# Kernel optimization log

Measured on AMD Instinct MI355X. Metric: run time of the kernel, lower is better.

Reference implementation:

```python
import jax, jax.numpy as jnp
import numpy as np

TAU = 2.0
THR = 1.0
ALPHA = 10.0
FLOW_SCALE = 16.0  # 2 ** flow_scale_pow2 (=4)
DECAY = 1.0 - 1.0 / TAU


def conv2d(x, w, b=None, stride=1, pad=0):
    # x: [N,C,H,W], w: [O,I,kh,kw]
    out = jax.lax.conv_general_dilated(
        x, w, (stride, stride), [(pad, pad), (pad, pad)],
        dimension_numbers=('NCHW', 'OIHW', 'NCHW'))
    if b is not None:
        out = out + b[None, :, None, None]
    return out


@jax.custom_vjp
def spike(v):
    return (v > 0).astype(v.dtype)

def _spike_fwd(v):
    return (v > 0).astype(v.dtype), v

def _spike_bwd(v, g):
    s = jax.nn.sigmoid(ALPHA * v)
    return (g * ALPHA * s * (1.0 - s),)

spike.defvjp(_spike_fwd, _spike_bwd)


def lif(x, w, b, mem, stride, pad):
    """Conv + leaky-integrate-fire with soft reset. mem init 0 -> first step mem=cur."""
    cur = conv2d(x, w, b, stride, pad)
    mem = mem * DECAY + cur
    s = spike(mem - THR)
    mem = mem - s * THR
    return s, mem


def up2(x):
    return jnp.repeat(jnp.repeat(x, 2, axis=2), 2, axis=3)


def forward(x, w_e1, b_e1, w_e2, b_e2, w_e3, b_e3, w_d3, b_d3,
            w_d2, b_d2, w_d1, b_d1, w_skip2, w_skip1, w_flow, b_flow):
    N, T, C, H, W = x.shape
    bc = w_e1.shape[0]  # base_ch = 32
    z = lambda c, h, w: jnp.zeros((N, c, h, w), x.dtype)
    init = (
        z(bc, H // 2, W // 2),      # mem_e1
        z(2 * bc, H // 4, W // 4),  # mem_e2
        z(4 * bc, H // 8, W // 8),  # mem_e3
        z(2 * bc, H // 4, W // 4),  # mem_d3
        z(bc, H // 2, W // 2),      # mem_d2
        z(bc, H, W),                # mem_d1
        z(bc, H // 2, W // 2),      # mean_e1 (zeros + /(t+1) rule == None-init)
        z(2 * bc, H // 4, W // 4),  # mean_e2
        z(2, H, W),                 # flow_mean
    )

    def step(carry, inp):
        t, xt = inp
        m1, m2, m3, md3, md2, md1, me1, me2, fm = carry
        s1, m1 = lif(xt, w_e1, b_e1, m1, 2, 2)
        s2, m2 = lif(s1, w_e2, b_e2, m2, 2, 1)
        s3, m3 = lif(s2, w_e3, b_e3, m3, 2, 1)
        tf = (t + 1).astype(xt.dtype)
        me1 = me1 + (s1 - me1) / tf
        me2 = me2 + (s2 - me2) / tf
        d3, md3 = lif(up2(s3), w_d3, b_d3, md3, 1, 1)
        d3 = d3 + conv2d(me2, w_skip2)
        d2, md2 = lif(up2(d3), w_d2, b_d2, md2, 1, 1)
        d2 = d2 + conv2d(me1, w_skip1)
        d1, md1 = lif(up2(d2), w_d1, b_d1, md1, 1, 1)
        flow = conv2d(d1, w_flow, b_flow, 1, 1) * FLOW_SCALE
        fm = fm + (flow - fm) / tf
        return (m1, m2, m3, md3, md2, md1, me1, me2, fm), flow

    _, flows = jax.lax.scan(step, init, (jnp.arange(T), jnp.moveaxis(x, 1, 0)))
    return flows[-1]  # return_last_flow=True -> flow of final timestep [N,2,H,W]


def setup_inputs() -> dict:
    key = jax.random.key(0)
    ks = jax.random.split(key, 16)
    N, T, H, W, bc = 4, 8, 256, 256, 32

    def w(k, o, i, kh, kw):
        return jax.random.normal(k, (o, i, kh, kw), jnp.float32) / np.sqrt(i * kh * kw)

    return {
        'x': jax.random.uniform(ks[0], (N, T, 2, H, W), jnp.float32),
        'w_e1': w(ks[1], bc, 2, 5, 5), 'b_e1': jnp.zeros((bc,), jnp.float32),
        'w_e2': w(ks[2], 2 * bc, bc, 3, 3), 'b_e2': jnp.zeros((2 * bc,), jnp.float32),
        'w_e3': w(ks[3], 4 * bc, 2 * bc, 3, 3), 'b_e3': jnp.zeros((4 * bc,), jnp.float32),
        'w_d3': w(ks[4], 2 * bc, 4 * bc, 3, 3), 'b_d3': jnp.zeros((2 * bc,), jnp.float32),
        'w_d2': w(ks[5], bc, 2 * bc, 3, 3), 'b_d2': jnp.zeros((bc,), jnp.float32),
        'w_d1': w(ks[6], bc, bc, 3, 3), 'b_d1': jnp.zeros((bc,), jnp.float32),
        'w_skip2': w(ks[7], 2 * bc, 2 * bc, 1, 1),
        'w_skip1': w(ks[8], bc, bc, 1, 1),
        'w_flow': w(ks[9], 2, bc, 3, 3), 'b_flow': jnp.zeros((2,), jnp.float32),
    }


def reference(x, w_e1, b_e1, w_e2, b_e2, w_e3, b_e3, w_d3, b_d3,
              w_d2, b_d2, w_d1, b_d1, w_skip2, w_skip1, w_flow, b_flow):
    return forward(x, w_e1, b_e1, w_e2, b_e2, w_e3, b_e3, w_d3, b_d3,
                   w_d2, b_d2, w_d1, b_d1, w_skip2, w_skip1, w_flow, b_flow)
```

## Files before the change

### kernel.cpp

```cpp
#include <hip/hip_runtime.h>
#include <cstdint>
#include <cstddef>


static constexpr float THRc   = 1.0f;
static constexpr float DECAYc = 0.5f;

__global__ __launch_bounds__(256) void prep_collapse(const float* __restrict__ w,
                                                     float* __restrict__ wc, int pairs)
{
    int idx = blockIdx.x * 256 + threadIdx.x;
    if (idx >= pairs) return;
    float a[3][3];
#pragma unroll
    for (int i = 0; i < 3; ++i)
#pragma unroll
        for (int j = 0; j < 3; ++j) a[i][j] = w[idx * 9 + i * 3 + j];
    float rs[2][2][3];
#pragma unroll
    for (int kx = 0; kx < 3; ++kx) {
        rs[0][0][kx] = a[0][kx];
        rs[0][1][kx] = a[1][kx] + a[2][kx];
        rs[1][0][kx] = a[0][kx] + a[1][kx];
        rs[1][1][kx] = a[2][kx];
    }
#pragma unroll
    for (int py = 0; py < 2; ++py)
#pragma unroll
        for (int px = 0; px < 2; ++px)
#pragma unroll
            for (int r = 0; r < 2; ++r) {
                float c0, c1;
                if (px == 0) { c0 = rs[py][r][0];               c1 = rs[py][r][1] + rs[py][r][2]; }
                else         { c0 = rs[py][r][0] + rs[py][r][1]; c1 = rs[py][r][2]; }
                wc[idx * 16 + ((py * 2 + px) * 2 + r) * 2 + 0] = c0;
                wc[idx * 16 + ((py * 2 + px) * 2 + r) * 2 + 1] = c1;
            }
}

template<int IC, int ICC, int OC, int SIH, int SIW, int CPT, int YPB, int OCT, int SKIP_IC>
__global__ __launch_bounds__(256) void dec_conv(
    const float* __restrict__ in,
    const float* __restrict__ wc,
    const float* __restrict__ bias,
    float* __restrict__ mem,
    float* __restrict__ out,
    const float* __restrict__ skip_in,
    const float* __restrict__ skip_w)
{
    constexpr int LPT  = SIW / CPT;
    static_assert(LPT * YPB == 64, "wave must tile the band");
    static_assert((ICC & (ICC - 1)) == 0, "ICC pow2");
    constexpr int OC_B = 4 * OCT;
    constexpr int NOCB = OC / OC_B;
    constexpr int NYB  = SIH / YPB;
    constexpr int SP   = SIW + 8;
    constexpr int SR   = YPB + 2;
    constexpr int OH   = 2 * SIH, OW = 2 * SIW;
    constexpr int NCH  = IC / ICC;
    constexpr int W4   = SIW / 4;

    __shared__ float sb[SR][ICC][SP];

    int b = blockIdx.x;
    const int ocb = b % NOCB; b /= NOCB;
    const int yb  = b % NYB;  b /= NYB;
    const int n   = b;
    const int y0  = yb * YPB;

    const int lane = threadIdx.x & 63;
    const int wav  = threadIdx.x >> 6;
    const int cl   = lane % LPT;
    const int yp   = lane / LPT;
    const int c0   = cl * CPT;
    const int y    = y0 + yp;

    const int oc0 = __builtin_amdgcn_readfirstlane(ocb * OC_B + wav * OCT);

    for (int f = threadIdx.x; f < SR * ICC * 2; f += 256) {
        int side = f & 1;
        int t    = f >> 1;
        int ic   = t & (ICC - 1);
        int r    = t / ICC;
        sb[r][ic][side ? (SIW + 4) : 3] = 0.0f;
    }

    float acc[OCT][2][2 * CPT];
#pragma unroll
    for (int j = 0; j < OCT; ++j) {
        float bv = bias[oc0 + j];
#pragma unroll
        for (int py = 0; py < 2; ++py)
#pragma unroll
            for (int q = 0; q < 2 * CPT; ++q) acc[j][py][q] = bv;
    }

    const float* inn = in + (size_t)n * IC * SIH * SIW;

    for (int ch = 0; ch < NCH; ++ch) {
        __syncthreads();
        const float* inb = inn + (size_t)ch * ICC * SIH * SIW;
        constexpr int SLOTS = SR * ICC * W4;
        for (int f = threadIdx.x; f < SLOTS; f += 256) {
            int c4 = f & (W4 - 1);
            int t  = f / W4;
            int ic = t & (ICC - 1);
            int r  = t / ICC;
            int sy = y0 - 1 + r;
            float4 v = make_float4(0.f, 0.f, 0.f, 0.f);
            if (sy >= 0 && sy < SIH)
                v = *reinterpret_cast<const float4*>(
                        inb + (size_t)ic * SIH * SIW + (size_t)sy * SIW + 4 * c4);
            *reinterpret_cast<float4*>(&sb[r][ic][4 + 4 * c4]) = v;
        }
        __syncthreads();
        for (int ic = 0; ic < ICC; ++ic) {
            float s[3][CPT + 2];
#pragma unroll
            for (int r = 0; r < 3; ++r)
#pragma unroll
                for (int k = 0; k < CPT + 2; ++k)
                    s[r][k] = sb[yp + r][ic][3 + c0 + k];
            const float* wp = wc + ((size_t)oc0 * IC + ch * ICC + ic) * 16;
#pragma unroll
            for (int j = 0; j < OCT; ++j) {
                float wv[16];
#pragma unroll
                for (int k = 0; k < 16; ++k) wv[k] = wp[(size_t)j * IC * 16 + k];
#pragma unroll
                for (int py = 0; py < 2; ++py)
#pragma unroll
                    for (int cc = 0; cc < CPT; ++cc)
#pragma unroll
                        for (int px = 0; px < 2; ++px) {
                            float v = acc[j][py][cc * 2 + px];
#pragma unroll
                            for (int rr = 0; rr < 2; ++rr)
#pragma unroll
                                for (int c2 = 0; c2 < 2; ++c2)
                                    v += wv[(py * 2 + px) * 4 + rr * 2 + c2]
                                       * s[py + rr][cc + px + c2];
                            acc[j][py][cc * 2 + px] = v;
                        }
            }
        }
    }

    float sk[OCT][2][2 * CPT] = {};
    if constexpr (SKIP_IC > 0) {
        const float* skn = skip_in + (size_t)n * SKIP_IC * OH * OW;
        for (int ic = 0; ic < SKIP_IC; ++ic) {
            float sval[2][2 * CPT];
#pragma unroll
            for (int py = 0; py < 2; ++py) {
                const float* srow = skn + ((size_t)ic * OH + (2 * y + py)) * OW + 2 * c0;
#pragma unroll
                for (int q = 0; q < 2 * CPT; ++q) sval[py][q] = srow[q];
            }
#pragma unroll
            for (int j = 0; j < OCT; ++j) {
                float wv = skip_w[(size_t)(oc0 + j) * SKIP_IC + ic];
#pragma unroll
                for (int py = 0; py < 2; ++py)
#pragma unroll
                    for (int q = 0; q < 2 * CPT; ++q) sk[j][py][q] += wv * sval[py][q];
            }
        }
    }

    const bool wout = (out != nullptr);
#pragma unroll
    for (int j = 0; j < OCT; ++j)
#pragma unroll
        for (int py = 0; py < 2; ++py) {
            size_t ob = (((size_t)n * OC + oc0 + j) * OH + (2 * y + py)) * OW + 2 * c0;
#pragma unroll
            for (int q = 0; q < 2 * CPT; ++q) {
                float m  = mem[ob + q] * DECAYc + acc[j][py][q];
                float sp = (m - THRc) > 0.0f ? 1.0f : 0.0f;
                mem[ob + q] = m - sp * THRc;
                if (wout) out[ob + q] = sp + sk[j][py][q];
            }
        }
}

template<int IC, int ICC, int OC, int IH, int IW, int K, int CPT, int LPT, int OCT, bool DO_MEAN>
__global__ __launch_bounds__(256) void enc_conv(
    const float* __restrict__ in, int in_nstride,
    const float* __restrict__ wgt,
    const float* __restrict__ bias,
    float* __restrict__ mem,
    float* __restrict__ out,
    float* __restrict__ mean,
    float inv_tf)
{
    constexpr int P    = K / 2;
    constexpr int OH   = IH / 2, OW = IW / 2;
    constexpr int SPr  = 4 + IW + P;
    constexpr int SP   = (SPr + 3) & ~3;
    constexpr int OC_B = 4 * OCT;
    constexpr int NOCB = OC / OC_B;
    constexpr int RL   = 2 * CPT + 2 * P - 1;
    constexpr int NCH  = IC / ICC;
    constexpr int W4   = IW / 4;
    static_assert(LPT * CPT == OW, "lanes x CPT must cover OW");
    static_assert((ICC & (ICC - 1)) == 0, "ICC pow2");

    __shared__ float sb[K][ICC][SP];

    int b = blockIdx.x;
    const int ocb = b % NOCB; b /= NOCB;
    const int y   = b % OH;   b /= OH;
    const int n   = b;

    const int lane = threadIdx.x & 63;
    const int wav  = threadIdx.x >> 6;
    const int x0   = (lane % LPT) * CPT;
    const int oc0  = __builtin_amdgcn_readfirstlane(ocb * OC_B + wav * OCT);

    for (int f = threadIdx.x; f < K * ICC * 2 * P; f += 256) {
        int h  = f % (2 * P);
        int t  = f / (2 * P);
        int ic = t & (ICC - 1);
        int r  = t / ICC;
        int col = (h < P) ? (4 - P + h) : (4 + IW + h - P);
        sb[r][ic][col] = 0.0f;
    }

    float acc[OCT][CPT];
#pragma unroll
    for (int j = 0; j < OCT; ++j) {
        float bv = bias[oc0 + j];
#pragma unroll
        for (int cc = 0; cc < CPT; ++cc) acc[j][cc] = bv;
    }

    const float* inn = in + (size_t)n * (size_t)in_nstride;

    for (int ch = 0; ch < NCH; ++ch) {
        __syncthreads();
        const float* inb = inn + (size_t)ch * ICC * IH * IW;
        constexpr int SLOTS = K * ICC * W4;
        for (int f = threadIdx.x; f < SLOTS; f += 256) {
            int c4 = f & (W4 - 1);
            int t  = f / W4;
            int ic = t & (ICC - 1);
            int r  = t / ICC;
            int sy = 2 * y - P + r;
            float4 v = make_float4(0.f, 0.f, 0.f, 0.f);
            if (sy >= 0 && sy < IH)
                v = *reinterpret_cast<const float4*>(
                        inb + (size_t)ic * IH * IW + (size_t)sy * IW + 4 * c4);
            *reinterpret_cast<float4*>(&sb[r][ic][4 + 4 * c4]) = v;
        }
        __syncthreads();
        for (int ic = 0; ic < ICC; ++ic) {
            float s[K][RL];
#pragma unroll
            for (int r = 0; r < K; ++r)
#pragma unroll
                for (int k = 0; k < RL; ++k)
                    s[r][k] = sb[r][ic][4 - P + 2 * x0 + k];
            const float* wp = wgt + ((size_t)oc0 * IC + ch * ICC + ic) * (K * K);
#pragma unroll
            for (int j = 0; j < OCT; ++j) {
                float wv[K * K];
#pragma unroll
                for (int k = 0; k < K * K; ++k) wv[k] = wp[(size_t)j * IC * K * K + k];
#pragma unroll
                for (int cc = 0; cc < CPT; ++cc)
#pragma unroll
                    for (int ky = 0; ky < K; ++ky)
#pragma unroll
                        for (int kx = 0; kx < K; ++kx)
                            acc[j][cc] += wv[ky * K + kx] * s[ky][2 * cc + kx];
            }
        }
    }

    if (lane < LPT) {
#pragma unroll
        for (int j = 0; j < OCT; ++j) {
            size_t ob = (((size_t)n * OC + oc0 + j) * OH + y) * OW + x0;
#pragma unroll
            for (int cc = 0; cc < CPT; ++cc) {
                float m  = mem[ob + cc] * DECAYc + acc[j][cc];
                float sp = (m - THRc) > 0.0f ? 1.0f : 0.0f;
                mem[ob + cc] = m - sp * THRc;
                if constexpr (DO_MEAN) {
                    float mv = mean[ob + cc];
                    mean[ob + cc] = mv + (sp - mv) * inv_tf;
                }
                out[ob + cc] = sp;
            }
        }
    }
}

template<int IC, int OC, int IH, int IW, int OH, int OW,
         int K, int STRIDE, int PAD, bool UP2, int SKIP_IC,
         bool DO_LIF, bool DO_MEAN>
__global__ __launch_bounds__(256) void conv_fused(
    const float* __restrict__ in, int in_nstride,
    const float* __restrict__ wgt,
    const float* __restrict__ bias,
    float* __restrict__ mem,
    float* __restrict__ out,
    const float* __restrict__ skip_in,
    const float* __restrict__ skip_w,
    float* __restrict__ mean,
    float inv_tf, float outscale)
{
    constexpr int VEC  = 4;
    constexpr int OWV  = OW / VEC;
    constexpr int WSZ  = IC * K * K;
    constexpr int SIH  = UP2 ? IH / 2 : IH;
    constexpr int SIW  = UP2 ? IW / 2 : IW;
    constexpr int RLEN = (VEC - 1) * STRIDE + K;

    __shared__ float sw[WSZ];

    const int bstart = blockIdx.x * 256;
    const int oc = (bstart / (OH * OWV)) % OC;

    for (int i = threadIdx.x; i < WSZ; i += 256) sw[i] = wgt[oc * WSZ + i];
    __syncthreads();

    const int idx = bstart + threadIdx.x;
    const int wx  = idx % OWV;
    int tt        = idx / OWV;
    const int oy  = tt % OH; tt /= OH;
    tt /= OC;
    const int n   = tt;
    const int ox0 = wx * VEC;

    const float bv = bias ? bias[oc] : 0.0f;
    float acc[VEC];
#pragma unroll
    for (int v = 0; v < VEC; ++v) acc[v] = bv;

    const float* inn = in + (size_t)n * (size_t)in_nstride;

    for (int ic = 0; ic < IC; ++ic) {
        const float* inc = inn + (size_t)ic * (SIH * SIW);
#pragma unroll
        for (int ky = 0; ky < K; ++ky) {
            const int uy = oy * STRIDE + ky - PAD;
            const bool rowok = (uy >= 0) & (uy < IH);
            int sy = UP2 ? (uy >> 1) : uy;
            sy = sy < 0 ? 0 : (sy > SIH - 1 ? SIH - 1 : sy);
            const float* __restrict__ row = inc + (size_t)sy * SIW;

            float r[RLEN];
#pragma unroll
            for (int j = 0; j < RLEN; ++j) {
                const int ux = ox0 * STRIDE - PAD + j;
                const bool ok = rowok & (ux >= 0) & (ux < IW);
                int sx = UP2 ? (ux >> 1) : ux;
                sx = sx < 0 ? 0 : (sx > SIW - 1 ? SIW - 1 : sx);
                r[j] = ok ? row[sx] : 0.0f;
            }
#pragma unroll
            for (int kx = 0; kx < K; ++kx) {
                const float wv = sw[(ic * K + ky) * K + kx];
#pragma unroll
                for (int v = 0; v < VEC; ++v)
                    acc[v] += r[v * STRIDE + kx] * wv;
            }
        }
    }

    const size_t obase = ((((size_t)n * OC + oc) * OH) + oy) * (size_t)OW + ox0;
#pragma unroll
    for (int v = 0; v < VEC; ++v) out[obase + v] = acc[v] * outscale;
}

extern "C" void kernel_launch(void* const* d_in, const int* in_sizes, int n_in,
                              void* d_out, int out_size, void* d_ws, size_t ws_size,
                              hipStream_t stream)
{
    const float* x     = (const float*)d_in[0];
    const float* w_e1  = (const float*)d_in[1];
    const float* b_e1  = (const float*)d_in[2];
    const float* w_e2  = (const float*)d_in[3];
    const float* b_e2  = (const float*)d_in[4];
    const float* w_e3  = (const float*)d_in[5];
    const float* b_e3  = (const float*)d_in[6];
    const float* w_d3  = (const float*)d_in[7];
    const float* b_d3  = (const float*)d_in[8];
    const float* w_d2  = (const float*)d_in[9];
    const float* b_d2  = (const float*)d_in[10];
    const float* w_d1  = (const float*)d_in[11];
    const float* b_d1  = (const float*)d_in[12];
    const float* w_sk2 = (const float*)d_in[13];
    const float* w_sk1 = (const float*)d_in[14];
    const float* w_fl  = (const float*)d_in[15];
    const float* b_fl  = (const float*)d_in[16];
    float* outp = (float*)d_out;

    float* ws = (float*)d_ws;
    size_t off = 0;
    auto alloc = [&](size_t nelem) { float* p = ws + off; off += nelem; return p; };

    float* m1  = alloc(4UL * 32 * 128 * 128);
    float* m2  = alloc(4UL * 64 * 64 * 64);
    float* m3  = alloc(4UL * 128 * 32 * 32);
    float* md3 = alloc(4UL * 64 * 64 * 64);
    float* md2 = alloc(4UL * 32 * 128 * 128);
    float* md1 = alloc(4UL * 32 * 256 * 256);
    float* me1 = alloc(4UL * 32 * 128 * 128);
    float* me2 = alloc(4UL * 64 * 64 * 64);
    const size_t zcount = off;
    float* s1  = alloc(4UL * 32 * 128 * 128);
    float* s2  = alloc(4UL * 64 * 64 * 64);
    float* s3  = alloc(4UL * 128 * 32 * 32);
    float* d3a = alloc(4UL * 64 * 64 * 64);
    float* d2a = alloc(4UL * 32 * 128 * 128);
    float* d1a = alloc(4UL * 32 * 256 * 256);
    float* wc3 = alloc(64UL * 128 * 16);
    float* wc2 = alloc(32UL * 64 * 16);
    float* wc1 = alloc(32UL * 32 * 16);
    (void)ws_size; (void)in_sizes; (void)n_in; (void)out_size;

    hipMemsetAsync(d_ws, 0, zcount * sizeof(float), stream);

    prep_collapse<<<(64 * 128 + 255) / 256, 256, 0, stream>>>(w_d3, wc3, 64 * 128);
    prep_collapse<<<(32 * 64 + 255) / 256, 256, 0, stream>>>(w_d2, wc2, 32 * 64);
    prep_collapse<<<(32 * 32 + 255) / 256, 256, 0, stream>>>(w_d1, wc1, 32 * 32);

    for (int t = 0; t < 8; ++t) {
        const float inv_tf = 1.0f / (float)(t + 1);
        const float* xt = x + (size_t)t * 2 * 256 * 256;

        enc_conv<2, 2, 32, 256, 256, 5, 2, 64, 2, true>
            <<<4 * 128 * 4, 256, 0, stream>>>(xt, 8 * 2 * 256 * 256, w_e1, b_e1,
                                              m1, s1, me1, inv_tf);
        enc_conv<32, 16, 64, 128, 128, 3, 1, 64, 2, true>
            <<<4 * 64 * 8, 256, 0, stream>>>(s1, 32 * 128 * 128, w_e2, b_e2,
                                             m2, s2, me2, inv_tf);
        enc_conv<64, 32, 128, 64, 64, 3, 1, 32, 4, false>
            <<<4 * 32 * 8, 256, 0, stream>>>(s2, 64 * 64 * 64, w_e3, b_e3,
                                             m3, s3, nullptr, inv_tf);
        dec_conv<128, 32, 64, 32, 32, 1, 2, 1, 64>
            <<<4 * 16 * 16, 256, 0, stream>>>(s3, wc3, b_d3, md3, d3a, me2, w_sk2);
        dec_conv<64, 16, 32, 64, 64, 1, 1, 1, 32>
            <<<4 * 64 * 8, 256, 0, stream>>>(d3a, wc2, b_d2, md2, d2a, me1, w_sk1);
        dec_conv<32, 16, 32, 128, 128, 2, 1, 2, 0>
            <<<4 * 128 * 4, 256, 0, stream>>>(d2a, wc1, b_d1, md1,
                                              (t == 7) ? d1a : nullptr, nullptr, nullptr);
        if (t == 7) {
            conv_fused<32, 2, 256, 256, 256, 256, 3, 1, 1, false, 0, false, false>
                <<<512, 256, 0, stream>>>(d1a, 32 * 256 * 256, w_fl, b_fl,
                                          nullptr, outp, nullptr, nullptr, nullptr, inv_tf, 16.0f);
        }
    }
}
```

Measured before the change: 2.399 ms.

## Stage conv weights and skip inputs in LDS instead of global loads

Encoder and decoder conv kernels now copy each input-channel chunk's weights into shared memory next to the input tile, so the inner loop reads weights from LDS with vector loads instead of scalar global loads. The decoder skip 1x1 conv now stages chunks of the skip input rows in shared memory with coalesced float4 loads, reusing the input-tile buffer. Channel chunk sizes are reduced for several layers to keep the larger shared footprint within limits. This adds extra syncs and LDS traffic and may change occupancy.

```diff
diff --git a/kernel.cpp b/kernel.cpp
--- a/kernel.cpp
+++ b/kernel.cpp
@@ -38,7 +38,8 @@
             }
 }
 
-template<int IC, int ICC, int OC, int SIH, int SIW, int CPT, int YPB, int OCT, int SKIP_IC>
+template<int IC, int ICC, int OC, int SIH, int SIW, int CPT, int YPB, int OCT,
+         int SKIP_IC, int SKC>
 __global__ __launch_bounds__(256) void dec_conv(
     const float* __restrict__ in,
     const float* __restrict__ wc,
@@ -59,8 +60,15 @@
     constexpr int OH   = 2 * SIH, OW = 2 * SIW;
     constexpr int NCH  = IC / ICC;
     constexpr int W4   = SIW / 4;
-
-    __shared__ float sb[SR][ICC][SP];
+    constexpr int TILE = SR * ICC * SP;
+    constexpr int WTSZ = OC_B * ICC * 16;
+    constexpr int OROWS = 2 * YPB;
+    constexpr int SKTILE = (SKIP_IC > 0) ? SKC * OROWS * OW : 0;
+    constexpr int BASE = TILE > SKTILE ? TILE : SKTILE;
+
+    __shared__ __align__(16) float smem[BASE + WTSZ];
+    float* const sb = smem;
+    float* const wt = smem + BASE;
 
     int b = blockIdx.x;
     const int ocb = b % NOCB; b /= NOCB;
@@ -82,7 +90,7 @@
         int t    = f >> 1;
         int ic   = t & (ICC - 1);
         int r    = t / ICC;
-        sb[r][ic][side ? (SIW + 4) : 3] = 0.0f;
+        sb[(r * ICC + ic) * SP + (side ? (SIW + 4) : 3)] = 0.0f;
     }
 
     float acc[OCT][2][2 * CPT];
@@ -111,7 +119,16 @@
             if (sy >= 0 && sy < SIH)
                 v = *reinterpret_cast<const float4*>(
                         inb + (size_t)ic * SIH * SIW + (size_t)sy * SIW + 4 * c4);
-            *reinterpret_cast<float4*>(&sb[r][ic][4 + 4 * c4]) = v;
+            *reinterpret_cast<float4*>(&sb[(r * ICC + ic) * SP + 4 + 4 * c4]) = v;
+        }
+        for (int f = threadIdx.x; f < WTSZ / 4; f += 256) {
+            int j   = f / (ICC * 4);
+            int rem = f % (ICC * 4);
+            int ic  = rem >> 2;
+            int k4  = rem & 3;
+            *reinterpret_cast<float4*>(&wt[f * 4]) =
+                *reinterpret_cast<const float4*>(
+                    wc + ((size_t)(ocb * OC_B + j) * IC + ch * ICC + ic) * 16 + 4 * k4);
         }
         __syncthreads();
         for (int ic = 0; ic < ICC; ++ic) {
@@ -120,13 +137,16 @@
             for (int r = 0; r < 3; ++r)
 #pragma unroll
                 for (int k = 0; k < CPT + 2; ++k)
-                    s[r][k] = sb[yp + r][ic][3 + c0 + k];
-            const float* wp = wc + ((size_t)oc0 * IC + ch * ICC + ic) * 16;
+                    s[r][k] = sb[((yp + r) * ICC + ic) * SP + 3 + c0 + k];
 #pragma unroll
             for (int j = 0; j < OCT; ++j) {
-                float wv[16];
-#pragma unroll
-                for (int k = 0; k < 16; ++k) wv[k] = wp[(size_t)j * IC * 16 + k];
+                const float* wl = wt + ((wav * OCT + j) * ICC + ic) * 16;
+                float4 w0 = *reinterpret_cast<const float4*>(wl + 0);
+                float4 w1 = *reinterpret_cast<const float4*>(wl + 4);
+                float4 w2 = *reinterpret_cast<const float4*>(wl + 8);
+                float4 w3 = *reinterpret_cast<const float4*>(wl + 12);
+                const float wv[16] = {w0.x, w0.y, w0.z, w0.w, w1.x, w1.y, w1.z, w1.w,
+                                      w2.x, w2.y, w2.z, w2.w, w3.x, w3.y, w3.z, w3.w};
 #pragma unroll
                 for (int py = 0; py < 2; ++py)
 #pragma unroll
@@ -149,22 +169,37 @@
     float sk[OCT][2][2 * CPT] = {};
     if constexpr (SKIP_IC > 0) {
         const float* skn = skip_in + (size_t)n * SKIP_IC * OH * OW;
-        for (int ic = 0; ic < SKIP_IC; ++ic) {
-            float sval[2][2 * CPT];
-#pragma unroll
-            for (int py = 0; py < 2; ++py) {
-                const float* srow = skn + ((size_t)ic * OH + (2 * y + py)) * OW + 2 * c0;
-#pragma unroll
-                for (int q = 0; q < 2 * CPT; ++q) sval[py][q] = srow[q];
-            }
-#pragma unroll
-            for (int j = 0; j < OCT; ++j) {
-                float wv = skip_w[(size_t)(oc0 + j) * SKIP_IC + ic];
+        constexpr int NSK = SKIP_IC / SKC;
+        constexpr int OW4 = OW / 4;
+        for (int sc = 0; sc < NSK; ++sc) {
+            __syncthreads();
+            for (int f = threadIdx.x; f < SKC * OROWS * OW4; f += 256) {
+                int c4 = f % OW4;
+                int t  = f / OW4;
+                int r  = t % OROWS;
+                int ic = t / OROWS;
+                *reinterpret_cast<float4*>(&sb[(ic * OROWS + r) * OW + 4 * c4]) =
+                    *reinterpret_cast<const float4*>(
+                        skn + ((size_t)(sc * SKC + ic) * OH + 2 * y0 + r) * OW + 4 * c4);
+            }
+            __syncthreads();
+            float wsk[OCT][SKC];
+#pragma unroll
+            for (int j = 0; j < OCT; ++j)
+#pragma unroll
+                for (int ic = 0; ic < SKC; ++ic)
+                    wsk[j][ic] = skip_w[(size_t)(oc0 + j) * SKIP_IC + sc * SKC + ic];
+#pragma unroll
+            for (int ic = 0; ic < SKC; ++ic)
 #pragma unroll
                 for (int py = 0; py < 2; ++py)
 #pragma unroll
-                    for (int q = 0; q < 2 * CPT; ++q) sk[j][py][q] += wv * sval[py][q];
-            }
+                    for (int q = 0; q < 2 * CPT; ++q) {
+                        float sval = sb[(ic * OROWS + 2 * yp + py) * OW + 2 * c0 + q];
+#pragma unroll
+                        for (int j = 0; j < OCT; ++j)
+                            sk[j][py][q] += wsk[j][ic] * sval;
+                    }
         }
     }
 
@@ -203,10 +238,15 @@
     constexpr int RL   = 2 * CPT + 2 * P - 1;
     constexpr int NCH  = IC / ICC;
     constexpr int W4   = IW / 4;
+    constexpr int KK   = K * K;
+    constexpr int TILE = K * ICC * SP;
+    constexpr int WTSZ = OC_B * ICC * KK;
     static_assert(LPT * CPT == OW, "lanes x CPT must cover OW");
     static_assert((ICC & (ICC - 1)) == 0, "ICC pow2");
 
-    __shared__ float sb[K][ICC][SP];
+    __shared__ __align__(16) float smem[TILE + WTSZ];
+    float* const sb = smem;
+    float* const wt = smem + TILE;
 
     int b = blockIdx.x;
     const int ocb = b % NOCB; b /= NOCB;
@@ -224,7 +264,7 @@
         int ic = t & (ICC - 1);
         int r  = t / ICC;
         int col = (h < P) ? (4 - P + h) : (4 + IW + h - P);
-        sb[r][ic][col] = 0.0f;
+        sb[(r * ICC + ic) * SP + col] = 0.0f;
     }
 
     float acc[OCT][CPT];
@@ -251,7 +291,14 @@
             if (sy >= 0 && sy < IH)
                 v = *reinterpret_cast<const float4*>(
                         inb + (size_t)ic * IH * IW + (size_t)sy * IW + 4 * c4);
-            *reinterpret_cast<float4*>(&sb[r][ic][4 + 4 * c4]) = v;
+            *reinterpret_cast<float4*>(&sb[(r * ICC + ic) * SP + 4 + 4 * c4]) = v;
+        }
+        for (int f = threadIdx.x; f < WTSZ; f += 256) {
+            int k  = f % KK;
+            int t  = f / KK;
+            int ic = t & (ICC - 1);
+            int j  = t / ICC;
+            wt[f] = wgt[((size_t)(ocb * OC_B + j) * IC + ch * ICC + ic) * KK + k];
         }
         __syncthreads();
         for (int ic = 0; ic < ICC; ++ic) {
@@ -260,13 +307,13 @@
             for (int r = 0; r < K; ++r)
 #pragma unroll
                 for (int k = 0; k < RL; ++k)
-                    s[r][k] = sb[r][ic][4 - P + 2 * x0 + k];
-            const float* wp = wgt + ((size_t)oc0 * IC + ch * ICC + ic) * (K * K);
+                    s[r][k] = sb[(r * ICC + ic) * SP + 4 - P + 2 * x0 + k];
 #pragma unroll
             for (int j = 0; j < OCT; ++j) {
-                float wv[K * K];
-#pragma unroll
-                for (int k = 0; k < K * K; ++k) wv[k] = wp[(size_t)j * IC * K * K + k];
+                const float* wl = wt + ((wav * OCT + j) * ICC + ic) * KK;
+                float wv[KK];
+#pragma unroll
+                for (int k = 0; k < KK; ++k) wv[k] = wl[k];
 #pragma unroll
                 for (int cc = 0; cc < CPT; ++cc)
 #pragma unroll
@@ -435,17 +482,17 @@
         enc_conv<2, 2, 32, 256, 256, 5, 2, 64, 2, true>
             <<<4 * 128 * 4, 256, 0, stream>>>(xt, 8 * 2 * 256 * 256, w_e1, b_e1,
                                               m1, s1, me1, inv_tf);
-        enc_conv<32, 16, 64, 128, 128, 3, 1, 64, 2, true>
+        enc_conv<32, 8, 64, 128, 128, 3, 1, 64, 2, true>
             <<<4 * 64 * 8, 256, 0, stream>>>(s1, 32 * 128 * 128, w_e2, b_e2,
                                              m2, s2, me2, inv_tf);
-        enc_conv<64, 32, 128, 64, 64, 3, 1, 32, 4, false>
+        enc_conv<64, 16, 128, 64, 64, 3, 1, 32, 4, false>
             <<<4 * 32 * 8, 256, 0, stream>>>(s2, 64 * 64 * 64, w_e3, b_e3,
                                              m3, s3, nullptr, inv_tf);
-        dec_conv<128, 32, 64, 32, 32, 1, 2, 1, 64>
+        dec_conv<128, 32, 64, 32, 32, 1, 2, 1, 64, 16>
             <<<4 * 16 * 16, 256, 0, stream>>>(s3, wc3, b_d3, md3, d3a, me2, w_sk2);
-        dec_conv<64, 16, 32, 64, 64, 1, 1, 1, 32>
+        dec_conv<64, 16, 32, 64, 64, 1, 1, 1, 32, 16>
             <<<4 * 64 * 8, 256, 0, stream>>>(d3a, wc2, b_d2, md2, d2a, me1, w_sk1);
-        dec_conv<32, 16, 32, 128, 128, 2, 1, 2, 0>
+        dec_conv<32, 8, 32, 128, 128, 2, 1, 2, 0, 1>
             <<<4 * 128 * 4, 256, 0, stream>>>(d2a, wc1, b_d1, md1,
                                               (t == 7) ? d1a : nullptr, nullptr, nullptr);
         if (t == 7) {
```

Measured after the change: 3.238 ms. 35.0% more time.
